# Optimization experiments

Measured on AMD Instinct MI355X. Metric: run time of the kernel, lower is better.

## Reference

```python
import jax, jax.numpy as jnp
import numpy as np


def setup_inputs() -> dict:
    key = jax.random.key(0)
    ks = jax.random.split(key, 6)
    B, N, D, A = 4, 512, 768, 128
    matrix = jax.random.normal(ks[0], (B, N, D), dtype=jnp.float32)
    mask = jax.random.randint(ks[1], (B, N, N, 1), 0, 2, dtype=jnp.int32)
    W1_w = jax.random.normal(ks[2], (D, A), dtype=jnp.float32) * (1.0 / np.sqrt(D))
    W1_b = jnp.zeros((A,), dtype=jnp.float32)
    W2_w = jax.random.normal(ks[3], (D, A), dtype=jnp.float32) * (1.0 / np.sqrt(D))
    W2_b = jnp.zeros((A,), dtype=jnp.float32)
    v_w = jax.random.normal(ks[4], (A, 1), dtype=jnp.float32) * (1.0 / np.sqrt(A))
    return {"matrix": matrix, "mask": mask, "W1_w": W1_w, "W1_b": W1_b,
            "W2_w": W2_w, "W2_b": W2_b, "v_w": v_w}


def reference(matrix, mask, W1_w, W1_b, W2_w, W2_b, v_w):
    # matrix: [B,N,D]; mask: [B,N,N,1]
    w1 = matrix @ W1_w + W1_b                     # [B,N,A] (query-side proj)
    w2 = matrix @ W2_w + W2_b                     # [B,N,A] (key-side proj)
    # pairwise additive scores: v . tanh(w1_i + w2_j) -> [B,N,N]
    pair = jnp.tanh(w1[:, :, None, :] + w2[:, None, :, :])  # [B,N,N,A]
    scores = jnp.einsum('bija,ao->bij', pair, v_w)           # [B,N,N]
    boolean_mask = mask[..., 0].astype(bool)                  # [B,N,N]
    neg = jnp.finfo(scores.dtype).min
    masked = jnp.where(boolean_mask, scores, neg)
    attn = jax.nn.softmax(masked, axis=-1)
    attn = jnp.where(jnp.isnan(attn), jnp.zeros((), attn.dtype), attn)
    return attn @ matrix                          # [B,N,D]
```

## Files before the change

kernel.cpp:

```cpp
#include <hip/hip_runtime.h>

#define B_ 4
#define N_ 512
#define D_ 768
#define A_ 128

typedef short bf16x8 __attribute__((ext_vector_type(8)));
typedef ushort u16x8 __attribute__((ext_vector_type(8)));
typedef ushort u16x4 __attribute__((ext_vector_type(4)));
typedef float f32x4 __attribute__((ext_vector_type(4)));

__device__ __forceinline__ ushort f2h(float x) {
  uint u = __builtin_bit_cast(uint, x);
  return (ushort)((u + 0x7fffu + ((u >> 16) & 1u)) >> 16);
}
__device__ __forceinline__ float h2f(ushort h) {
  uint u = ((uint)h) << 16;
  return __builtin_bit_cast(float, u);
}
__device__ __forceinline__ bf16x8 ld8(const ushort* p) {
  return *(const bf16x8*)p;
}
#define MFMA(a, b, c) __builtin_amdgcn_mfma_f32_16x16x32_bf16(a, b, c, 0, 0, 0)

__global__ __launch_bounds__(256) void k0_prep(
    const float* __restrict__ M, const float* __restrict__ W1,
    const float* __restrict__ W2, const float* __restrict__ vw,
    ushort* __restrict__ Mr_h, ushort* __restrict__ Mr_l,
    ushort* __restrict__ Mt_h, ushort* __restrict__ Mt_l,
    ushort* __restrict__ Wt_h, ushort* __restrict__ Wt_l,
    float* __restrict__ uvec) {
  __shared__ ushort lds_h[64][40];
  __shared__ ushort lds_l[64][40];
  const int t = threadIdx.x;
  const int bid = blockIdx.x;
  if (bid < 768) {
    const int dq = bid % 12;
    const int rest = bid / 12;
    const int d0 = dq * 64;
    const int n0 = (rest & 15) * 32;
    const int b = rest >> 4;
    const int n = t >> 3;
    const int dg = (t & 7) * 8;
    const size_t roff = ((size_t)(b * N_ + n0 + n)) * D_ + d0 + dg;
    const float4 v0 = *(const float4*)(M + roff);
    const float4 v1 = *(const float4*)(M + roff + 4);
    const float x[8] = {v0.x, v0.y, v0.z, v0.w, v1.x, v1.y, v1.z, v1.w};
    u16x8 vh, vl;
#pragma unroll
    for (int e = 0; e < 8; ++e) {
      ushort h = f2h(x[e]);
      ushort l = f2h(x[e] - h2f(h));
      vh[e] = h;
      vl[e] = l;
      lds_h[dg + e][n] = h;
      lds_l[dg + e][n] = l;
    }
    *(u16x8*)(Mr_h + roff) = vh;
    *(u16x8*)(Mr_l + roff) = vl;
    __syncthreads();
    const int dd = t >> 2;
    const int ng = (t & 3) * 8;
    const size_t toff = ((size_t)b * D_ + d0 + dd) * N_ + n0 + ng;
    *(u16x8*)(Mt_h + toff) = *(const u16x8*)(&lds_h[dd][ng]);
    *(u16x8*)(Mt_l + toff) = *(const u16x8*)(&lds_l[dd][ng]);
  } else {
    const int c = t;
    const int k0 = (bid - 768) * 8;
    const float* __restrict__ Wp = (c < A_) ? W1 : W2;
    const int cc = c & (A_ - 1);
    u16x8 vh, vl;
#pragma unroll
    for (int e = 0; e < 8; ++e) {
      float x = Wp[(size_t)(k0 + e) * A_ + cc];
      ushort h = f2h(x);
      vh[e] = h;
      vl[e] = f2h(x - h2f(h));
    }
    *(u16x8*)(Wt_h + (size_t)c * D_ + k0) = vh;
    *(u16x8*)(Wt_l + (size_t)c * D_ + k0) = vl;
    if (bid == 768 && c < A_) uvec[c] = -2.f * vw[c];
  }
}

__global__ __launch_bounds__(256) void k1_mfma(
    const ushort* __restrict__ Mr_h, const ushort* __restrict__ Mr_l,
    const ushort* __restrict__ Wt_h, const ushort* __restrict__ Wt_l,
    const float* __restrict__ b1, const float* __restrict__ b2,
    float* __restrict__ w1e, ushort* __restrict__ w2e) {
  __shared__ float l_red[4][32][33];
  const int t = threadIdx.x;
  const int l = t & 63;
  const int w = t >> 6;
  const int r = l & 15, g = l >> 4;
  const int row0 = blockIdx.x * 32;
  const int cb = blockIdx.y * 32;
  const int kbase = w * 192;
  const size_t oA = (size_t)(row0 + r) * D_ + kbase + g * 8;
  const size_t oA2 = oA + (size_t)16 * D_;
  const size_t oB = (size_t)(cb + r) * D_ + kbase + g * 8;
  const size_t oB2 = oB + (size_t)16 * D_;
  f32x4 acc[2][2] = {};
  bf16x8 A[2][4], Bv[2][4];
#define K1LOAD(s, k0)                                                        \
  A[s][0] = ld8(Mr_h + oA + (k0));  A[s][1] = ld8(Mr_h + oA2 + (k0));        \
  A[s][2] = ld8(Mr_l + oA + (k0));  A[s][3] = ld8(Mr_l + oA2 + (k0));        \
  Bv[s][0] = ld8(Wt_h + oB + (k0)); Bv[s][1] = ld8(Wt_h + oB2 + (k0));       \
  Bv[s][2] = ld8(Wt_l + oB + (k0)); Bv[s][3] = ld8(Wt_l + oB2 + (k0));
#define K1MM(s)                                                              \
  acc[0][0] = MFMA(A[s][0], Bv[s][0], acc[0][0]);                            \
  acc[0][0] = MFMA(A[s][0], Bv[s][2], acc[0][0]);                            \
  acc[0][0] = MFMA(A[s][2], Bv[s][0], acc[0][0]);                            \
  acc[0][1] = MFMA(A[s][0], Bv[s][1], acc[0][1]);                            \
  acc[0][1] = MFMA(A[s][0], Bv[s][3], acc[0][1]);                            \
  acc[0][1] = MFMA(A[s][2], Bv[s][1], acc[0][1]);                            \
  acc[1][0] = MFMA(A[s][1], Bv[s][0], acc[1][0]);                            \
  acc[1][0] = MFMA(A[s][1], Bv[s][2], acc[1][0]);                            \
  acc[1][0] = MFMA(A[s][3], Bv[s][0], acc[1][0]);                            \
  acc[1][1] = MFMA(A[s][1], Bv[s][1], acc[1][1]);                            \
  acc[1][1] = MFMA(A[s][1], Bv[s][3], acc[1][1]);                            \
  acc[1][1] = MFMA(A[s][3], Bv[s][1], acc[1][1]);
  K1LOAD(0, 0)
#pragma unroll
  for (int kt = 0; kt < 6; ++kt) {
    if (kt & 1) {
      if (kt < 5) { K1LOAD(0, (kt + 1) * 32) }
      K1MM(1)
    } else {
      if (kt < 5) { K1LOAD(1, (kt + 1) * 32) }
      K1MM(0)
    }
  }
#undef K1LOAD
#undef K1MM
#pragma unroll
  for (int fi = 0; fi < 2; ++fi)
#pragma unroll
    for (int fj = 0; fj < 2; ++fj)
#pragma unroll
      for (int rr = 0; rr < 4; ++rr)
        l_red[w][fi * 16 + g * 4 + rr][fj * 16 + r] = acc[fi][fj][rr];
  __syncthreads();

  const float SC = 2.8853900817779268f;
  const int b = row0 >> 9;
  const int n0 = row0 & (N_ - 1);
  if (cb < A_) {
#pragma unroll
    for (int k = 0; k < 4; ++k) {
      const int row = (t >> 5) + k * 8;
      const int col = t & 31;
      float v = l_red[0][row][col] + l_red[1][row][col] +
                l_red[2][row][col] + l_red[3][row][col];
      v = (v + b1[cb + col]) * SC;
      w1e[(size_t)(row0 + row) * A_ + cb + col] = __builtin_amdgcn_exp2f(v);
    }
  } else {
#pragma unroll
    for (int k = 0; k < 4; ++k) {
      const int row = t & 31;
      const int col = (t >> 5) + k * 8;
      float v = l_red[0][row][col] + l_red[1][row][col] +
                l_red[2][row][col] + l_red[3][row][col];
      v = (v + b2[cb - A_ + col]) * SC;
      w2e[(size_t)(b * A_ + cb - A_ + col) * N_ + n0 + row] =
          f2h(__builtin_amdgcn_exp2f(v));
    }
  }
}

__global__ __launch_bounds__(512) void k2_scores(
    const float* __restrict__ w1e, const ushort* __restrict__ w2e,
    const float* __restrict__ uvec, const int* __restrict__ mask,
    const float* __restrict__ vw, ushort* __restrict__ ah,
    ushort* __restrict__ al) {
  __shared__ ushort l_w2[2][16][N_];
  __shared__ float l_red[4][2];
  __shared__ float l_sum[4][2];
  const int t = threadIdx.x;
  const int lane = t & 63;
  const int w = t >> 6;
  const int r = w >> 1;
  const int h = w & 1;
  const int i0 = blockIdx.x * 4;
  const int b = i0 >> 9;
  const int i = i0 + r;
  const int iu = __builtin_amdgcn_readfirstlane(i);
  const float* __restrict__ w1row = w1e + (size_t)iu * A_;

  float vs = vw[lane] + vw[64 + lane];
#pragma unroll
  for (int off = 32; off; off >>= 1) vs += __shfl_xor(vs, off);

  const ushort* __restrict__ w2src = w2e + (size_t)b * A_ * N_;
  u16x8 st[2];

#define STAGE_LOAD(cc)                                                      \
  {                                                                         \
    const ushort* __restrict__ src = w2src + (size_t)(cc) * 16 * N_;        \
    _Pragma("unroll") for (int k = 0; k < 2; ++k) {                         \
      const int f = t + k * 512;                                            \
      st[k] = *(const u16x8*)(src + (size_t)(f >> 6) * N_ + (f & 63) * 8);  \
    }                                                                       \
  }
#define STAGE_WRITE(bf)                                                     \
  {                                                                         \
    _Pragma("unroll") for (int k = 0; k < 2; ++k) {                         \
      const int f = t + k * 512;                                            \
      *(u16x8*)(&l_w2[bf][f >> 6][(f & 63) * 8]) = st[k];                   \
    }                                                                       \
  }

  STAGE_LOAD(0)
  STAGE_WRITE(0)
  __syncthreads();

  const int jb = h * 256 + lane * 4;
  float4 s = {0.f, 0.f, 0.f, 0.f};
#pragma unroll 1
  for (int cc = 0; cc < 8; ++cc) {
    if (cc + 1 < 8) STAGE_LOAD(cc + 1)
    const ushort(*wb)[N_] = l_w2[cc & 1];
#pragma unroll 1
    for (int aa = 0; aa < 4; ++aa) {
      const float4 wa = *(const float4*)(w1row + cc * 16 + aa * 4);
      const float4 uu = *(const float4*)(uvec + cc * 16 + aa * 4);
      const float wa_[4] = {wa.x, wa.y, wa.z, wa.w};
      const float uu_[4] = {uu.x, uu.y, uu.z, uu.w};
#pragma unroll
      for (int e = 0; e < 4; ++e) {
        const float wx = wa_[e];
        const float ux = uu_[e];
        const u16x4 xr = *(const u16x4*)(&wb[aa * 4 + e][jb]);
        s.x = fmaf(ux, __builtin_amdgcn_rcpf(fmaf(wx, h2f(xr[0]), 1.f)), s.x);
        s.y = fmaf(ux, __builtin_amdgcn_rcpf(fmaf(wx, h2f(xr[1]), 1.f)), s.y);
        s.z = fmaf(ux, __builtin_amdgcn_rcpf(fmaf(wx, h2f(xr[2]), 1.f)), s.z);
        s.w = fmaf(ux, __builtin_amdgcn_rcpf(fmaf(wx, h2f(xr[3]), 1.f)), s.w);
      }
    }
    if (cc + 1 < 8) { STAGE_WRITE((cc + 1) & 1) }
    __syncthreads();
  }
#undef STAGE_LOAD
#undef STAGE_WRITE

  const float NEG = -3.402823466e38f;
  const int4 mk = *(const int4*)(mask + (size_t)i * N_ + jb);
  s.x = mk.x ? (vs + s.x) : NEG;
  s.y = mk.y ? (vs + s.y) : NEG;
  s.z = mk.z ? (vs + s.z) : NEG;
  s.w = mk.w ? (vs + s.w) : NEG;

  float rmax = fmaxf(fmaxf(s.x, s.y), fmaxf(s.z, s.w));
#pragma unroll
  for (int off = 32; off; off >>= 1) rmax = fmaxf(rmax, __shfl_xor(rmax, off));
  if (lane == 0) l_red[r][h] = rmax;
  __syncthreads();
  rmax = fmaxf(l_red[r][0], l_red[r][1]);

  const float L2E = 1.4426950408889634f;
  s.x = __builtin_amdgcn_exp2f((s.x - rmax) * L2E);
  s.y = __builtin_amdgcn_exp2f((s.y - rmax) * L2E);
  s.z = __builtin_amdgcn_exp2f((s.z - rmax) * L2E);
  s.w = __builtin_amdgcn_exp2f((s.w - rmax) * L2E);
  float psum = (s.x + s.y) + (s.z + s.w);
#pragma unroll
  for (int off = 32; off; off >>= 1) psum += __shfl_xor(psum, off);
  if (lane == 0) l_sum[r][h] = psum;
  __syncthreads();
  const float inv = __builtin_amdgcn_rcpf(l_sum[r][0] + l_sum[r][1]);

  const float p[4] = {s.x * inv, s.y * inv, s.z * inv, s.w * inv};
  u16x4 vh, vl;
#pragma unroll
  for (int e = 0; e < 4; ++e) {
    const ushort hh = f2h(p[e]);
    vh[e] = hh;
    vl[e] = f2h(p[e] - h2f(hh));
  }
  *(u16x4*)(ah + (size_t)i * N_ + jb) = vh;
  *(u16x4*)(al + (size_t)i * N_ + jb) = vl;
}

__global__ __launch_bounds__(256) void k3_mfma(
    const ushort* __restrict__ ah, const ushort* __restrict__ al,
    const ushort* __restrict__ Mt_h, const ushort* __restrict__ Mt_l,
    float* __restrict__ out) {
  __shared__ float l_red[4][64][33];
  const int t = threadIdx.x;
  const int l = t & 63;
  const int w = t >> 6;
  const int r = l & 15, g = l >> 4;
  const int row0 = blockIdx.x * 64;
  const int d0 = blockIdx.y * 32;
  const int b = row0 >> 9;
  const int jbase = w * 128;
  const ushort* __restrict__ Bh = Mt_h + (size_t)b * D_ * N_;
  const ushort* __restrict__ Bl = Mt_l + (size_t)b * D_ * N_;
  size_t oA[4];
#pragma unroll
  for (int fi = 0; fi < 4; ++fi)
    oA[fi] = (size_t)(row0 + fi * 16 + r) * N_ + jbase + g * 8;
  const size_t oB = (size_t)(d0 + r) * N_ + jbase + g * 8;
  const size_t oB2 = oB + (size_t)16 * N_;
  f32x4 acc[4][2] = {};
  bf16x8 A[2][8], Bv[2][4];
#define K3LOAD(s, j0)                                                        \
  A[s][0] = ld8(ah + oA[0] + (j0)); A[s][1] = ld8(ah + oA[1] + (j0));        \
  A[s][2] = ld8(ah + oA[2] + (j0)); A[s][3] = ld8(ah + oA[3] + (j0));        \
  A[s][4] = ld8(al + oA[0] + (j0)); A[s][5] = ld8(al + oA[1] + (j0));        \
  A[s][6] = ld8(al + oA[2] + (j0)); A[s][7] = ld8(al + oA[3] + (j0));        \
  Bv[s][0] = ld8(Bh + oB + (j0));   Bv[s][1] = ld8(Bh + oB2 + (j0));         \
  Bv[s][2] = ld8(Bl + oB + (j0));   Bv[s][3] = ld8(Bl + oB2 + (j0));
#define K3MM(s)                                                              \
  _Pragma("unroll") for (int fi = 0; fi < 4; ++fi)                           \
  _Pragma("unroll") for (int fd = 0; fd < 2; ++fd) {                         \
    acc[fi][fd] = MFMA(A[s][fi], Bv[s][fd], acc[fi][fd]);                    \
    acc[fi][fd] = MFMA(A[s][fi], Bv[s][fd + 2], acc[fi][fd]);                \
    acc[fi][fd] = MFMA(A[s][fi + 4], Bv[s][fd], acc[fi][fd]);                \
  }
  K3LOAD(0, 0)
#pragma unroll
  for (int kt = 0; kt < 4; ++kt) {
    if (kt & 1) {
      if (kt < 3) { K3LOAD(0, (kt + 1) * 32) }
      K3MM(1)
    } else {
      if (kt < 3) { K3LOAD(1, (kt + 1) * 32) }
      K3MM(0)
    }
  }
#undef K3LOAD
#undef K3MM
#pragma unroll
  for (int fi = 0; fi < 4; ++fi)
#pragma unroll
    for (int fd = 0; fd < 2; ++fd)
#pragma unroll
      for (int rr = 0; rr < 4; ++rr)
        l_red[w][fi * 16 + g * 4 + rr][fd * 16 + r] = acc[fi][fd][rr];
  __syncthreads();
#pragma unroll
  for (int k = 0; k < 8; ++k) {
    const int row = (t >> 5) + k * 8;
    const int col = t & 31;
    const float v = l_red[0][row][col] + l_red[1][row][col] +
                    l_red[2][row][col] + l_red[3][row][col];
    out[(size_t)(row0 + row) * D_ + d0 + col] = v;
  }
}

extern "C" void kernel_launch(void* const* d_in, const int* in_sizes, int n_in,
                              void* d_out, int out_size, void* d_ws,
                              size_t ws_size, hipStream_t stream) {
  const float* M = (const float*)d_in[0];
  const int* mask = (const int*)d_in[1];
  const float* W1 = (const float*)d_in[2];
  const float* b1 = (const float*)d_in[3];
  const float* W2 = (const float*)d_in[4];
  const float* b2 = (const float*)d_in[5];
  const float* vw = (const float*)d_in[6];
  float* out = (float*)d_out;

  float* w1e = (float*)d_ws;
  ushort* w2eb = (ushort*)(w1e + 2048 * A_);
  ushort* ah = w2eb + 4 * A_ * N_;
  ushort* al = ah + 2048 * N_;
  ushort* Mr_h = al + 2048 * N_;
  ushort* Mr_l = Mr_h + 2048 * D_;
  ushort* Mt_h = Mr_l + 2048 * D_;
  ushort* Mt_l = Mt_h + 2048 * D_;
  ushort* Wt_h = Mt_l + 2048 * D_;
  ushort* Wt_l = Wt_h + 256 * D_;
  float* uvec = (float*)(Wt_l + 256 * D_);

  k0_prep<<<864, 256, 0, stream>>>(M, W1, W2, vw, Mr_h, Mr_l, Mt_h, Mt_l,
                                   Wt_h, Wt_l, uvec);
  k1_mfma<<<dim3(2048 / 32, 8), 256, 0, stream>>>(Mr_h, Mr_l, Wt_h, Wt_l,
                                                  b1, b2, w1e, w2eb);
  k2_scores<<<(B_ * N_) / 4, 512, 0, stream>>>(w1e, w2eb, uvec, mask, vw,
                                               ah, al);
  k3_mfma<<<dim3(2048 / 64, D_ / 32), 256, 0, stream>>>(ah, al, Mt_h, Mt_l,
                                                        out);
}
```

Measured before the change: 66.99 us.

## Split each score row across four waves and halve rows per block

The score kernel now processes two query rows per 512-thread block, with four waves each covering 128 key columns and two scores per thread. The grid doubles and a launch-bounds occupancy hint is added, aiming at more parallelism and shorter per-thread dependency chains. In exchange, each LDS-staged w2 tile is reused by fewer rows, so the w2 global traffic and staging cost per row doubles.

```diff
diff --git a/kernel.cpp b/kernel.cpp
--- a/kernel.cpp
+++ b/kernel.cpp
@@ -169,20 +169,20 @@
   }
 }
 
-__global__ __launch_bounds__(512) void k2_scores(
+__global__ __launch_bounds__(512, 8) void k2_scores(
     const float* __restrict__ w1e, const ushort* __restrict__ w2e,
     const float* __restrict__ uvec, const int* __restrict__ mask,
     const float* __restrict__ vw, ushort* __restrict__ ah,
     ushort* __restrict__ al) {
   __shared__ ushort l_w2[2][16][N_];
-  __shared__ float l_red[4][2];
-  __shared__ float l_sum[4][2];
+  __shared__ float l_red[2][4];
+  __shared__ float l_sum[2][4];
   const int t = threadIdx.x;
   const int lane = t & 63;
   const int w = t >> 6;
-  const int r = w >> 1;
-  const int h = w & 1;
-  const int i0 = blockIdx.x * 4;
+  const int r = w >> 2;
+  const int q = w & 3;
+  const int i0 = blockIdx.x * 2;
   const int b = i0 >> 9;
   const int i = i0 + r;
   const int iu = __builtin_amdgcn_readfirstlane(i);
@@ -215,8 +215,8 @@
   STAGE_WRITE(0)
   __syncthreads();
 
-  const int jb = h * 256 + lane * 4;
-  float4 s = {0.f, 0.f, 0.f, 0.f};
+  const int jq = q * 128 + lane * 2;
+  float sx = 0.f, sy = 0.f;
 #pragma unroll 1
   for (int cc = 0; cc < 8; ++cc) {
     if (cc + 1 < 8) STAGE_LOAD(cc + 1)
@@ -231,11 +231,11 @@
       for (int e = 0; e < 4; ++e) {
         const float wx = wa_[e];
         const float ux = uu_[e];
-        const u16x4 xr = *(const u16x4*)(&wb[aa * 4 + e][jb]);
-        s.x = fmaf(ux, __builtin_amdgcn_rcpf(fmaf(wx, h2f(xr[0]), 1.f)), s.x);
-        s.y = fmaf(ux, __builtin_amdgcn_rcpf(fmaf(wx, h2f(xr[1]), 1.f)), s.y);
-        s.z = fmaf(ux, __builtin_amdgcn_rcpf(fmaf(wx, h2f(xr[2]), 1.f)), s.z);
-        s.w = fmaf(ux, __builtin_amdgcn_rcpf(fmaf(wx, h2f(xr[3]), 1.f)), s.w);
+        const uint xr = *(const uint*)(&wb[aa * 4 + e][jq]);
+        const float x0 = __builtin_bit_cast(float, xr << 16);
+        const float x1 = __builtin_bit_cast(float, xr & 0xffff0000u);
+        sx = fmaf(ux, __builtin_amdgcn_rcpf(fmaf(wx, x0, 1.f)), sx);
+        sy = fmaf(ux, __builtin_amdgcn_rcpf(fmaf(wx, x1, 1.f)), sy);
       }
     }
     if (cc + 1 < 8) { STAGE_WRITE((cc + 1) & 1) }
@@ -245,41 +245,38 @@
 #undef STAGE_WRITE
 
   const float NEG = -3.402823466e38f;
-  const int4 mk = *(const int4*)(mask + (size_t)i * N_ + jb);
-  s.x = mk.x ? (vs + s.x) : NEG;
-  s.y = mk.y ? (vs + s.y) : NEG;
-  s.z = mk.z ? (vs + s.z) : NEG;
-  s.w = mk.w ? (vs + s.w) : NEG;
-
-  float rmax = fmaxf(fmaxf(s.x, s.y), fmaxf(s.z, s.w));
+  const int2 mk = *(const int2*)(mask + (size_t)i * N_ + jq);
+  sx = mk.x ? (vs + sx) : NEG;
+  sy = mk.y ? (vs + sy) : NEG;
+
+  float rmax = fmaxf(sx, sy);
 #pragma unroll
   for (int off = 32; off; off >>= 1) rmax = fmaxf(rmax, __shfl_xor(rmax, off));
-  if (lane == 0) l_red[r][h] = rmax;
-  __syncthreads();
-  rmax = fmaxf(l_red[r][0], l_red[r][1]);
+  if (lane == 0) l_red[r][q] = rmax;
+  __syncthreads();
+  rmax = fmaxf(fmaxf(l_red[r][0], l_red[r][1]),
+               fmaxf(l_red[r][2], l_red[r][3]));
 
   const float L2E = 1.4426950408889634f;
-  s.x = __builtin_amdgcn_exp2f((s.x - rmax) * L2E);
-  s.y = __builtin_amdgcn_exp2f((s.y - rmax) * L2E);
-  s.z = __builtin_amdgcn_exp2f((s.z - rmax) * L2E);
-  s.w = __builtin_amdgcn_exp2f((s.w - rmax) * L2E);
-  float psum = (s.x + s.y) + (s.z + s.w);
+  sx = __builtin_amdgcn_exp2f((sx - rmax) * L2E);
+  sy = __builtin_amdgcn_exp2f((sy - rmax) * L2E);
+  float psum = sx + sy;
 #pragma unroll
   for (int off = 32; off; off >>= 1) psum += __shfl_xor(psum, off);
-  if (lane == 0) l_sum[r][h] = psum;
-  __syncthreads();
-  const float inv = __builtin_amdgcn_rcpf(l_sum[r][0] + l_sum[r][1]);
-
-  const float p[4] = {s.x * inv, s.y * inv, s.z * inv, s.w * inv};
-  u16x4 vh, vl;
-#pragma unroll
-  for (int e = 0; e < 4; ++e) {
-    const ushort hh = f2h(p[e]);
-    vh[e] = hh;
-    vl[e] = f2h(p[e] - h2f(hh));
-  }
-  *(u16x4*)(ah + (size_t)i * N_ + jb) = vh;
-  *(u16x4*)(al + (size_t)i * N_ + jb) = vl;
+  if (lane == 0) l_sum[r][q] = psum;
+  __syncthreads();
+  const float inv = __builtin_amdgcn_rcpf(
+      (l_sum[r][0] + l_sum[r][1]) + (l_sum[r][2] + l_sum[r][3]));
+
+  const float p0 = sx * inv;
+  const float p1 = sy * inv;
+  const ushort h0 = f2h(p0);
+  const ushort h1 = f2h(p1);
+  const ushort g0 = f2h(p0 - h2f(h0));
+  const ushort g1 = f2h(p1 - h2f(h1));
+  const size_t base = (size_t)i * N_ + jq;
+  *(uint*)(ah + base) = (uint)h0 | ((uint)h1 << 16);
+  *(uint*)(al + base) = (uint)g0 | ((uint)g1 << 16);
 }
 
 __global__ __launch_bounds__(256) void k3_mfma(
@@ -378,7 +375,7 @@
                                    Wt_h, Wt_l, uvec);
   k1_mfma<<<dim3(2048 / 32, 8), 256, 0, stream>>>(Mr_h, Mr_l, Wt_h, Wt_l,
                                                   b1, b2, w1e, w2eb);
-  k2_scores<<<(B_ * N_) / 4, 512, 0, stream>>>(w1e, w2eb, uvec, mask, vw,
+  k2_scores<<<(B_ * N_) / 2, 512, 0, stream>>>(w1e, w2eb, uvec, mask, vw,
                                                ah, al);
   k3_mfma<<<dim3(2048 / 64, D_ / 32), 256, 0, stream>>>(ah, al, Mt_h, Mt_l,
                                                         out);
```

Result: no change. 67.11 us (+0.2%).
